# Performance work log

Measured on AMD Instinct MI355X. Metric: run time of the kernel, lower is better.

## Reference

```python
import jax, jax.numpy as jnp
import numpy as np

E, H, B, S = 512, 8, 8, 1024  # embed_dim, n_head, batch, n_agent (sequence)
DH = E // H
DECAY_SCALING = 1.0


def _rmsnorm(x, scale, eps=1e-6):
    return x * jax.lax.rsqrt(jnp.mean(x * x, axis=-1, keepdims=True) + eps) * scale


def _groupnorm(y, scale, bias, n_head, eps=1e-5):
    # GroupNorm with num_groups = n_head over the feature axis (flax semantics).
    b, s, e = y.shape
    yg = y.reshape(b, s, n_head, e // n_head)
    mu = jnp.mean(yg, axis=-1, keepdims=True)
    var = jnp.var(yg, axis=-1, keepdims=True)
    yn = (yg - mu) * jax.lax.rsqrt(var + eps)
    return yn.reshape(b, s, e) * scale + bias


def _decay_kappas(n_head, scaling):
    # RetNet multi-scale decays: 1 - exp(linspace(log(1/32), log(1/512), H))
    k = 1.0 - jnp.exp(jnp.linspace(jnp.log(1.0 / 32.0), jnp.log(1.0 / 512.0), n_head))
    return (k * scaling).astype(jnp.float32)


def _msr(key_x, query_x, value_x, wq, wk, wv, wg, wo, gs, gb, kappas):
    # Parallel multi-scale retention (masked / causal, full_self_retention=False).
    b, s, e = query_x.shape
    h = wq.shape[0]
    q = jnp.einsum('bse,hed->bhsd', query_x, wq)
    k = jnp.einsum('bse,hed->bhsd', key_x, wk)
    v = jnp.einsum('bse,hed->bhsd', value_x, wv)
    n = jnp.arange(s)
    diff = n[:, None] - n[None, :]
    causal = diff >= 0
    expnt = jnp.where(causal, diff, 0).astype(q.dtype)
    # D[h,n,m] = kappa_h^(n-m) for n>=m else 0
    D = jnp.where(causal[None], kappas[:, None, None] ** expnt[None], 0.0)
    scores = jnp.einsum('bhnd,bhmd->bhnm', q, k) * D[None]  # [B,H,S,S]
    ret = jnp.einsum('bhnm,bhmd->bhnd', scores, v)
    ret = ret.transpose(0, 2, 1, 3).reshape(b, s, e)
    ret = _groupnorm(ret, gs, gb, h)
    return (jax.nn.swish(query_x @ wg) * ret) @ wo


def _swiglu(x, w_gate, w_lin, w_out):
    return (jax.nn.swish(x @ w_gate) * (x @ w_lin)) @ w_out


def setup_inputs() -> dict:
    key = jax.random.key(0)
    ks = jax.random.split(key, 20)
    sc = 0.02
    d = {
        'x': jax.random.normal(ks[0], (B, S, E), jnp.float32),
        'obs_rep': jax.random.normal(ks[1], (B, S, E), jnp.float32),
        # retention 1 params
        'wq1': jax.random.normal(ks[2], (H, E, DH), jnp.float32) * sc,
        'wk1': jax.random.normal(ks[3], (H, E, DH), jnp.float32) * sc,
        'wv1': jax.random.normal(ks[4], (H, E, DH), jnp.float32) * sc,
        'wg1': jax.random.normal(ks[5], (E, E), jnp.float32) * sc,
        'wo1': jax.random.normal(ks[6], (E, E), jnp.float32) * sc,
        'gs1': jnp.ones((E,), jnp.float32),
        'gb1': jnp.zeros((E,), jnp.float32),
        # retention 2 params
        'wq2': jax.random.normal(ks[7], (H, E, DH), jnp.float32) * sc,
        'wk2': jax.random.normal(ks[8], (H, E, DH), jnp.float32) * sc,
        'wv2': jax.random.normal(ks[9], (H, E, DH), jnp.float32) * sc,
        'wg2': jax.random.normal(ks[10], (E, E), jnp.float32) * sc,
        'wo2': jax.random.normal(ks[11], (E, E), jnp.float32) * sc,
        'gs2': jnp.ones((E,), jnp.float32),
        'gb2': jnp.zeros((E,), jnp.float32),
        # RMSNorm scales
        'ln1_s': jnp.ones((E,), jnp.float32),
        'ln2_s': jnp.ones((E,), jnp.float32),
        'ln3_s': jnp.ones((E,), jnp.float32),
        # SwiGLU(hidden=E, input=E)
        'ffn_w_lin': jax.random.normal(ks[12], (E, E), jnp.float32) * sc,
        'ffn_w_gate': jax.random.normal(ks[13], (E, E), jnp.float32) * sc,
        'ffn_w_out': jax.random.normal(ks[14], (E, E), jnp.float32) * sc,
    }
    return d


def reference(x, obs_rep, wq1, wk1, wv1, wg1, wo1, gs1, gb1,
              wq2, wk2, wv2, wg2, wo2, gs2, gb2,
              ln1_s, ln2_s, ln3_s, ffn_w_lin, ffn_w_gate, ffn_w_out):
    kappas = _decay_kappas(H, DECAY_SCALING)
    # x = ln1(x + retn1(key=x, query=x, value=x))
    x1 = _rmsnorm(x + _msr(x, x, x, wq1, wk1, wv1, wg1, wo1, gs1, gb1, kappas), ln1_s)
    # x = ln2(obs_rep + retn2(key=x1, query=obs_rep, value=x1))
    x2 = _rmsnorm(obs_rep + _msr(x1, obs_rep, x1, wq2, wk2, wv2, wg2, wo2, gs2, gb2, kappas), ln2_s)
    # out = ln3(x2 + ffn(x2))
    return _rmsnorm(x2 + _swiglu(x2, ffn_w_gate, ffn_w_lin, ffn_w_out), ln3_s)
```

## Files before the change

### kernel.cpp

```cpp
#include <hip/hip_runtime.h>
#include <hip/hip_bf16.h>
#include <stdint.h>

typedef unsigned short u16;
typedef unsigned int   u32;
typedef __bf16 bf16x8 __attribute__((ext_vector_type(8)));
typedef u16    u16x8  __attribute__((ext_vector_type(8)));
typedef float  f32x4  __attribute__((ext_vector_type(4)));

#define E_   512
#define H_   8
#define DH_  64
#define B_   8
#define S_   1024
#define M_   (B_ * S_)
#define NTOT (M_ * E_)

__device__ __forceinline__ u16 f2bf(float f) {
    u32 x = __float_as_uint(f);
    x += 0x7fffu + ((x >> 16) & 1u);
    return (u16)(x >> 16);
}
__device__ __forceinline__ float bf2f(u16 b) { return __uint_as_float((u32)b << 16); }
__device__ __forceinline__ bf16x8 as_bf(u16x8 v) {
    union { u16x8 u; bf16x8 b; } x; x.u = v; return x.b;
}
__device__ __forceinline__ u32 cvtpk(float lo, float hi) {
    u32 r;
    asm("v_cvt_pk_bf16_f32 %0, %1, %2" : "=v"(r) : "v"(lo), "v"(hi));
    return r;
}
__device__ __forceinline__ void gll16(const u16* g, u16* l) {
    __builtin_amdgcn_global_load_lds((const __attribute__((address_space(1))) u32*)g,
                                     (__attribute__((address_space(3))) u32*)l, 16, 0, 0);
}
__device__ __forceinline__ void xcd_map(int f, int nwg, int gx, int& bx, int& by) {
    int nf = (f & 7) * (nwg >> 3) + (f >> 3);
    bx = nf % gx; by = nf / gx;
}

__global__ __launch_bounds__(256) void prep_weights(
    const float* __restrict__ wq1, const float* __restrict__ wk1, const float* __restrict__ wv1,
    const float* __restrict__ wg1, const float* __restrict__ wq2, const float* __restrict__ wk2,
    const float* __restrict__ wv2, const float* __restrict__ wg2, const float* __restrict__ wgat,
    const float* __restrict__ wlin, const float* __restrict__ wo1, const float* __restrict__ wo2,
    const float* __restrict__ wout,
    u16* __restrict__ WC1, u16* __restrict__ WC2, u16* __restrict__ WF,
    u16* __restrict__ WO1t, u16* __restrict__ WO2t, u16* __restrict__ WOUt) {
    __shared__ float tle[64][65];
    const int rt = blockIdx.y, c0 = blockIdx.x * 64, tid = threadIdx.x;
    u16* dst; const float* src; int lr0; bool qkv = false; int nb0 = 0, h = 0;
    if (rt < 64) {
        bool s1 = rt < 32;
        dst = s1 ? WC1 : WC2;
        int r = (rt & 31) * 64; lr0 = r;
        if (r < 1536) {
            qkv = true; h = (r >> 6) & 7;
            src = (r < 512) ? (s1 ? wq1 : wq2) : (r < 1024) ? (s1 ? wk1 : wk2) : (s1 ? wv1 : wv2);
        } else { src = s1 ? wg1 : wg2; nb0 = r - 1536; }
    } else if (rt < 80) {
        dst = WF; int r = (rt - 64) * 64; lr0 = r;
        src = (r < 512) ? wgat : wlin; nb0 = r & 511;
    } else if (rt < 88) { dst = WO1t; lr0 = (rt - 80) * 64; src = wo1; nb0 = lr0; }
    else if (rt < 96)   { dst = WO2t; lr0 = (rt - 88) * 64; src = wo2; nb0 = lr0; }
    else                { dst = WOUt; lr0 = (rt - 96) * 64; src = wout; nb0 = lr0; }

    #pragma unroll
    for (int i = 0; i < 16; ++i) {
        int idx = i * 256 + tid, a = idx >> 6, b = idx & 63;
        tle[a][b] = qkv ? src[(size_t)(h * 512 + c0 + a) * 64 + b]
                        : src[(size_t)(c0 + a) * 512 + nb0 + b];
    }
    __syncthreads();
    #pragma unroll
    for (int i = 0; i < 16; ++i) {
        int idx = i * 256 + tid;
        dst[(size_t)(lr0 + (idx >> 6)) * 512 + c0 + (idx & 63)] = f2bf(tle[idx & 63][idx >> 6]);
    }
}

__global__ __launch_bounds__(256) void cvt_both(const float* __restrict__ x,
                                                const float* __restrict__ obs,
                                                u16* __restrict__ XB, u16* __restrict__ OB) {
    int i = blockIdx.x * 256 + threadIdx.x;
    float4 v = ((const float4*)x)[i];
    ushort4 o;
    o.x = f2bf(v.x); o.y = f2bf(v.y); o.z = f2bf(v.z); o.w = f2bf(v.w);
    ((ushort4*)XB)[i] = o;
    v = ((const float4*)obs)[i];
    o.x = f2bf(v.x); o.y = f2bf(v.y); o.z = f2bf(v.z); o.w = f2bf(v.w);
    ((ushort4*)OB)[i] = o;
}

__global__ __launch_bounds__(256) void gemm_qkvg(const u16* __restrict__ A1,
                                                 const u16* __restrict__ A2,
                                                 const u16* __restrict__ W,
                                                 u16* __restrict__ QB, u16* __restrict__ KB,
                                                 u16* __restrict__ VT, u16* __restrict__ GB) {
    __shared__ u16 Als[128 * 64];
    __shared__ u16 Bls[128 * 64];
    const int tid = threadIdx.x;
    const int l = tid & 63, w = tid >> 6;
    const int wm = w & 1, wn = w >> 1;
    int bx, by; xcd_map(blockIdx.x, 1024, 16, bx, by);
    const int bm = by * 128, bn = bx * 128;
    const int which = bx >> 2;
    const u16* A = (which == 1 || which == 2) ? A2 : A1;

    size_t srcA[4], srcB[4]; int ldst[4];
    #pragma unroll
    for (int c = 0; c < 4; ++c) {
        int row = c * 32 + w * 8 + (l >> 3);
        int chs = (l & 7) ^ (row & 7);
        srcA[c] = (size_t)(bm + row) * E_ + chs * 8;
        srcB[c] = (size_t)(bn + row) * E_ + chs * 8;
        ldst[c] = c * 2048 + w * 512;
    }
    int aoff[2][4], boff[2][4];
    #pragma unroll
    for (int kk = 0; kk < 2; ++kk)
        #pragma unroll
        for (int f = 0; f < 4; ++f) {
            int ra = wm * 64 + f * 16 + (l & 15);
            int rb = wn * 64 + f * 16 + (l & 15);
            int ch = kk * 4 + (l >> 4);
            aoff[kk][f] = ra * 128 + ((ch ^ (ra & 7)) << 4);
            boff[kk][f] = rb * 128 + ((ch ^ (rb & 7)) << 4);
        }

    f32x4 acc[4][4] = {};
    for (int t = 0; t < 8; ++t) {
        const int k1 = t * 64;
        #pragma unroll
        for (int c = 0; c < 4; ++c) {
            gll16(A + srcA[c] + k1, &Als[ldst[c]]);
            gll16(W + srcB[c] + k1, &Bls[ldst[c]]);
        }
        __syncthreads();
        #pragma unroll
        for (int kk = 0; kk < 2; ++kk) {
            bf16x8 af[4], bfr[4];
            #pragma unroll
            for (int f = 0; f < 4; ++f) {
                af[f]  = as_bf(*(const u16x8*)((const char*)Als + aoff[kk][f]));
                bfr[f] = as_bf(*(const u16x8*)((const char*)Bls + boff[kk][f]));
            }
            #pragma unroll
            for (int m = 0; m < 4; ++m)
                #pragma unroll
                for (int n = 0; n < 4; ++n)
                    acc[m][n] = __builtin_amdgcn_mfma_f32_16x16x32_bf16(af[m], bfr[n], acc[m][n], 0, 0, 0);
        }
        __syncthreads();
    }

    #pragma unroll
    for (int m = 0; m < 4; ++m) {
        int row = bm + wm * 64 + m * 16 + ((l >> 4) << 2);
        #pragma unroll
        for (int n = 0; n < 4; ++n) {
            int coll = (bn & 511) + wn * 64 + n * 16 + (l & 15);
            f32x4 v = acc[m][n];
            if (which == 2) {
                size_t va = (((size_t)(row >> 10) * 8 + (coll >> 6)) * 64 + (coll & 63)) * 1024
                            + (row & 1023);
                ushort4 o;
                o.x = f2bf(v[0]); o.y = f2bf(v[1]); o.z = f2bf(v[2]); o.w = f2bf(v[3]);
                *(ushort4*)(VT + va) = o;
            } else {
                u16* dst = (which == 0) ? QB : (which == 1) ? KB : GB;
                #pragma unroll
                for (int r = 0; r < 4; ++r) dst[(size_t)(row + r) * E_ + coll] = f2bf(v[r]);
            }
        }
    }
}

__global__ __launch_bounds__(256) void gemm_wo(const u16* __restrict__ A,
                                               const u16* __restrict__ W,
                                               float* __restrict__ Cf) {
    __shared__ u16 Als[64 * 64];
    __shared__ u16 Bls[128 * 64];
    const int tid = threadIdx.x;
    const int l = tid & 63, w = tid >> 6;
    const int wm = w & 1, wn = w >> 1;
    int bx, by; xcd_map(blockIdx.x, 512, 4, bx, by);
    const int bm = by * 64, bn = bx * 128;

    size_t srcA[2], srcB[4]; int ldstA[2], ldstB[4];
    #pragma unroll
    for (int c = 0; c < 4; ++c) {
        int row = c * 32 + w * 8 + (l >> 3);
        int chs = (l & 7) ^ (row & 7);
        if (c < 2) { srcA[c] = (size_t)(bm + row) * E_ + chs * 8; ldstA[c] = c * 2048 + w * 512; }
        srcB[c] = (size_t)(bn + row) * E_ + chs * 8;
        ldstB[c] = c * 2048 + w * 512;
    }
    int aoff[2][2], boff[2][4];
    #pragma unroll
    for (int kk = 0; kk < 2; ++kk) {
        #pragma unroll
        for (int f = 0; f < 2; ++f) {
            int ra = wm * 32 + f * 16 + (l & 15);
            aoff[kk][f] = ra * 128 + (((kk * 4 + (l >> 4)) ^ (ra & 7)) << 4);
        }
        #pragma unroll
        for (int f = 0; f < 4; ++f) {
            int rb = wn * 64 + f * 16 + (l & 15);
            boff[kk][f] = rb * 128 + (((kk * 4 + (l >> 4)) ^ (rb & 7)) << 4);
        }
    }

    f32x4 acc[2][4] = {};
    for (int t = 0; t < 8; ++t) {
        const int k1 = t * 64;
        #pragma unroll
        for (int c = 0; c < 2; ++c) gll16(A + srcA[c] + k1, &Als[ldstA[c]]);
        #pragma unroll
        for (int c = 0; c < 4; ++c) gll16(W + srcB[c] + k1, &Bls[ldstB[c]]);
        __syncthreads();
        #pragma unroll
        for (int kk = 0; kk < 2; ++kk) {
            bf16x8 af[2], bfr[4];
            #pragma unroll
            for (int f = 0; f < 2; ++f) af[f] = as_bf(*(const u16x8*)((const char*)Als + aoff[kk][f]));
            #pragma unroll
            for (int f = 0; f < 4; ++f) bfr[f] = as_bf(*(const u16x8*)((const char*)Bls + boff[kk][f]));
            #pragma unroll
            for (int m = 0; m < 2; ++m)
                #pragma unroll
                for (int n = 0; n < 4; ++n)
                    acc[m][n] = __builtin_amdgcn_mfma_f32_16x16x32_bf16(af[m], bfr[n], acc[m][n], 0, 0, 0);
        }
        __syncthreads();
    }

    #pragma unroll
    for (int m = 0; m < 2; ++m) {
        int row = bm + wm * 32 + m * 16 + ((l >> 4) << 2);
        #pragma unroll
        for (int n = 0; n < 4; ++n) {
            int col = bn + wn * 64 + n * 16 + (l & 15);
            f32x4 v = acc[m][n];
            #pragma unroll
            for (int r = 0; r < 4; ++r) Cf[(size_t)(row + r) * E_ + col] = v[r];
        }
    }
}

__global__ __launch_bounds__(256) void gemm_ffn(const u16* __restrict__ A,
                                                const u16* __restrict__ W,
                                                u16* __restrict__ T) {
    __shared__ u16 Als[64 * 64];
    __shared__ u16 Bgs[64 * 64];
    __shared__ u16 Bls[64 * 64];
    const int tid = threadIdx.x;
    const int l = tid & 63, w = tid >> 6;
    const int wm = w & 1, wn = w >> 1;
    int bx, by; xcd_map(blockIdx.x, 1024, 8, bx, by);
    const int bm = by * 64, bn = bx * 64;

    size_t srcA[2], srcG[2], srcL[2]; int ldst[2];
    #pragma unroll
    for (int c = 0; c < 2; ++c) {
        int row = c * 32 + w * 8 + (l >> 3);
        int chs = (l & 7) ^ (row & 7);
        srcA[c] = (size_t)(bm + row) * E_ + chs * 8;
        srcG[c] = (size_t)(bn + row) * E_ + chs * 8;
        srcL[c] = (size_t)(512 + bn + row) * E_ + chs * 8;
        ldst[c] = c * 2048 + w * 512;
    }
    int aoff[2][2], goff[2][2];
    #pragma unroll
    for (int kk = 0; kk < 2; ++kk)
        #pragma unroll
        for (int f = 0; f < 2; ++f) {
            int ra = wm * 32 + f * 16 + (l & 15);
            int rb = wn * 32 + f * 16 + (l & 15);
            aoff[kk][f] = ra * 128 + (((kk * 4 + (l >> 4)) ^ (ra & 7)) << 4);
            goff[kk][f] = rb * 128 + (((kk * 4 + (l >> 4)) ^ (rb & 7)) << 4);
        }

    f32x4 accg[2][2] = {}, accl[2][2] = {};
    for (int t = 0; t < 8; ++t) {
        const int k1 = t * 64;
        #pragma unroll
        for (int c = 0; c < 2; ++c) {
            gll16(A + srcA[c] + k1, &Als[ldst[c]]);
            gll16(W + srcG[c] + k1, &Bgs[ldst[c]]);
            gll16(W + srcL[c] + k1, &Bls[ldst[c]]);
        }
        __syncthreads();
        #pragma unroll
        for (int kk = 0; kk < 2; ++kk) {
            bf16x8 af[2], bg[2], bl[2];
            #pragma unroll
            for (int f = 0; f < 2; ++f) {
                af[f] = as_bf(*(const u16x8*)((const char*)Als + aoff[kk][f]));
                bg[f] = as_bf(*(const u16x8*)((const char*)Bgs + goff[kk][f]));
                bl[f] = as_bf(*(const u16x8*)((const char*)Bls + goff[kk][f]));
            }
            #pragma unroll
            for (int m = 0; m < 2; ++m)
                #pragma unroll
                for (int n = 0; n < 2; ++n) {
                    accg[m][n] = __builtin_amdgcn_mfma_f32_16x16x32_bf16(af[m], bg[n], accg[m][n], 0, 0, 0);
                    accl[m][n] = __builtin_amdgcn_mfma_f32_16x16x32_bf16(af[m], bl[n], accl[m][n], 0, 0, 0);
                }
        }
        __syncthreads();
    }

    #pragma unroll
    for (int m = 0; m < 2; ++m) {
        int row = bm + wm * 32 + m * 16 + ((l >> 4) << 2);
        #pragma unroll
        for (int n = 0; n < 2; ++n) {
            int col = bn + wn * 32 + n * 16 + (l & 15);
            #pragma unroll
            for (int r = 0; r < 4; ++r) {
                float g = accg[m][n][r], lv = accl[m][n][r];
                T[(size_t)(row + r) * E_ + col] = f2bf(g * lv / (1.f + __expf(-g)));
            }
        }
    }
}

__global__ __launch_bounds__(256) void retention_fused(
        const u16* __restrict__ Q, const u16* __restrict__ K,
        const u16* __restrict__ VT, const u16* __restrict__ G,
        const float* __restrict__ gs, const float* __restrict__ gb,
        u16* __restrict__ T) {
    __shared__ u16 Qs[128 * 64], Ks[128 * 64], Vts[64 * 128], Ps[128 * 128];
    const int tid = threadIdx.x;
    const int l = tid & 63, w = tid >> 6;
    int id = blockIdx.x, nb, bh;
    if (id < 256) { nb = id & 7; bh = id >> 3; }
    else { int j = id - 256; nb = 7 - (j & 7); bh = 32 + (j >> 3); }
    const int h = bh & 7;
    const int n0 = nb * 128;
    const size_t base = (size_t)(bh >> 3) * (S_ * E_) + h * DH_;

    const float kappa = 1.0f - __expf(-3.46573590f + (float)h * -0.39608410f);
    const float log2k = log2f(kappa);
    const float ik = 1.0f / kappa;
    const float ikp2 = ik * ik, ikp3 = ik * ik * ik;

    float gsv[4], gbv[4];
    #pragma unroll
    for (int fd = 0; fd < 4; ++fd) {
        gsv[fd] = gs[h * 64 + fd * 16 + (l & 15)];
        gbv[fd] = gb[h * 64 + fd * 16 + (l & 15)];
    }

    {
        #pragma unroll
        for (int c = 0; c < 4; ++c) {
            int row = c * 32 + w * 8 + (l >> 3);
            int chs = (l & 7) ^ (row & 7);
            gll16(Q + base + (size_t)(n0 + row) * E_ + chs * 8, &Qs[c * 2048 + w * 512]);
        }
    }
    __syncthreads();
    bf16x8 qf[2][2];
    #pragma unroll
    for (int kk = 0; kk < 2; ++kk)
        #pragma unroll
        for (int fn = 0; fn < 2; ++fn) {
            int row = w * 32 + fn * 16 + (l & 15);
            int ch = kk * 4 + (l >> 4);
            qf[kk][fn] = as_bf(*(const u16x8*)((const char*)Qs + row * 128 + ((ch ^ (row & 7)) << 4)));
        }

    f32x4 acc[2][4] = {};
    const int nmin = n0 + w * 32;
    const int nmax = nmin + 31;

    for (int t = 0; t <= nb; ++t) {
        const int m0 = t * 128;
        __syncthreads();
        #pragma unroll
        for (int c = 0; c < 4; ++c) {
            int row = c * 32 + w * 8 + (l >> 3);
            int chs = (l & 7) ^ (row & 7);
            gll16(K + base + (size_t)(m0 + row) * E_ + chs * 8, &Ks[c * 2048 + w * 512]);
            int d = c * 16 + w * 4 + (l >> 4);
            int vch = (l & 15) ^ (d & 7);
            gll16(VT + ((size_t)bh * 64 + d) * 1024 + m0 + vch * 8, &Vts[c * 2048 + w * 512]);
        }
        __syncthreads();
        if (m0 > nmax) continue;
        const bool inter = (nmin >= m0 + 127);

        #pragma unroll
        for (int fmh = 0; fmh < 2; ++fmh) {
            bf16x8 kf[2][4];
            #pragma unroll
            for (int kk = 0; kk < 2; ++kk)
                #pragma unroll
                for (int f = 0; f < 4; ++f) {
                    int row = (fmh * 4 + f) * 16 + (l & 15);
                    int ch = kk * 4 + (l >> 4);
                    kf[kk][f] = as_bf(*(const u16x8*)((const char*)Ks + row * 128 + ((ch ^ (row & 7)) << 4)));
                }
            f32x4 s[4][2] = {};
            __builtin_amdgcn_s_setprio(1);
            #pragma unroll
            for (int kk = 0; kk < 2; ++kk)
                #pragma unroll
                for (int f = 0; f < 4; ++f)
                    #pragma unroll
                    for (int fn = 0; fn < 2; ++fn)
                        s[f][fn] = __builtin_amdgcn_mfma_f32_16x16x32_bf16(kf[kk][f], qf[kk][fn], s[f][fn], 0, 0, 0);
            __builtin_amdgcn_s_setprio(0);

            #pragma unroll
            for (int f = 0; f < 4; ++f) {
                int fm = fmh * 4 + f;
                #pragma unroll
                for (int fn = 0; fn < 2; ++fn) {
                    int n_g  = n0 + w * 32 + fn * 16 + (l & 15);
                    int mb_g = m0 + fm * 16 + ((l >> 4) << 2);
                    int delta = n_g - mb_g;
                    float wb = exp2f((float)delta * log2k);
                    f32x4 v = s[f][fn];
                    float p0, p1, p2, p3;
                    if (inter) {
                        float w1 = wb * ik, w2 = w1 * ik, w3 = w2 * ik;
                        p0 = v[0] * wb; p1 = v[1] * w1; p2 = v[2] * w2; p3 = v[3] * w3;
                    } else {
                        p0 = (delta >= 0) ? v[0] * wb : 0.f;
                        p1 = (delta >= 1) ? v[1] * wb * ik : 0.f;
                        p2 = (delta >= 2) ? v[2] * wb * ikp2 : 0.f;
                        p3 = (delta >= 3) ? v[3] * wb * ikp3 : 0.f;
                    }
                    int nl  = w * 32 + fn * 16 + (l & 15);
                    int mbl = fm * 16 + ((l >> 4) << 2);
                    int byteoff = nl * 256 + ((((mbl >> 3)) ^ (nl & 7)) << 4) + ((mbl & 4) << 1);
                    uint2 pk;
                    pk.x = cvtpk(p0, p1);
                    pk.y = cvtpk(p2, p3);
                    *(uint2*)((char*)Ps + byteoff) = pk;
                }
            }
        }

        #pragma unroll
        for (int km = 0; km < 4; ++km) {
            bf16x8 pf[2];
            #pragma unroll
            for (int fn = 0; fn < 2; ++fn) {
                int row = w * 32 + fn * 16 + (l & 15);
                int ch = km * 4 + (l >> 4);
                pf[fn] = as_bf(*(const u16x8*)((const char*)Ps + row * 256 + ((ch ^ (row & 7)) << 4)));
            }
            __builtin_amdgcn_s_setprio(1);
            #pragma unroll
            for (int fd = 0; fd < 4; ++fd) {
                int d = fd * 16 + (l & 15);
                int mch = km * 4 + (l >> 4);
                bf16x8 vfr = as_bf(*(const u16x8*)((const char*)Vts + d * 256 + ((mch ^ (d & 7)) << 4)));
                #pragma unroll
                for (int fn = 0; fn < 2; ++fn)
                    acc[fn][fd] = __builtin_amdgcn_mfma_f32_16x16x32_bf16(pf[fn], vfr, acc[fn][fd], 0, 0, 0);
            }
            __builtin_amdgcn_s_setprio(0);
        }
    }

    #pragma unroll
    for (int fn = 0; fn < 2; ++fn) {
        #pragma unroll
        for (int r = 0; r < 4; ++r) {
            float s1 = 0.f, s2 = 0.f;
            #pragma unroll
            for (int fd = 0; fd < 4; ++fd) { float v = acc[fn][fd][r]; s1 += v; s2 += v * v; }
            #pragma unroll
            for (int off = 1; off < 16; off <<= 1) {
                s1 += __shfl_xor(s1, off, 64);
                s2 += __shfl_xor(s2, off, 64);
            }
            float mean = s1 * (1.f / 64.f);
            float var  = s2 * (1.f / 64.f) - mean * mean;
            float rinv = rsqrtf(var + 1e-5f);
            int rowg = n0 + w * 32 + fn * 16 + ((l >> 4) << 2) + r;
            size_t rb = base + (size_t)rowg * E_;
            #pragma unroll
            for (int fd = 0; fd < 4; ++fd) {
                int d = fd * 16 + (l & 15);
                float ny = (acc[fn][fd][r] - mean) * rinv;
                float rn = ny * gsv[fd] + gbv[fd];
                float g = bf2f(G[rb + d]);
                T[rb + d] = f2bf(g * rn / (1.f + __expf(-g)));
            }
        }
    }
}

__global__ __launch_bounds__(512) void rmsnorm_res(const float* __restrict__ Xf,
                                                   const u16* __restrict__ Xb,
                                                   const float* __restrict__ Y,
                                                   const float* __restrict__ sc,
                                                   float* __restrict__ outf,
                                                   u16* __restrict__ outb) {
    __shared__ float part[8];
    size_t row = blockIdx.x;
    int t = threadIdx.x;
    float xv = Xf ? Xf[row * E_ + t] : bf2f(Xb[row * E_ + t]);
    float v = xv + Y[row * E_ + t];
    float sq = v * v;
    #pragma unroll
    for (int off = 1; off < 64; off <<= 1) sq += __shfl_xor(sq, off, 64);
    if ((t & 63) == 0) part[t >> 6] = sq;
    __syncthreads();
    float tot = 0.0f;
    #pragma unroll
    for (int i = 0; i < 8; ++i) tot += part[i];
    float r = rsqrtf(tot * (1.0f / 512.0f) + 1e-6f);
    float o = v * r * sc[t];
    if (outf) outf[row * E_ + t] = o;
    if (outb) outb[row * E_ + t] = f2bf(o);
}

extern "C" void kernel_launch(void* const* d_in, const int* in_sizes, int n_in,
                              void* d_out, int out_size, void* d_ws, size_t ws_size,
                              hipStream_t stream) {
    const float* x    = (const float*)d_in[0];
    const float* obs  = (const float*)d_in[1];
    const float* wq1  = (const float*)d_in[2];
    const float* wk1  = (const float*)d_in[3];
    const float* wv1  = (const float*)d_in[4];
    const float* wg1  = (const float*)d_in[5];
    const float* wo1  = (const float*)d_in[6];
    const float* gs1  = (const float*)d_in[7];
    const float* gb1  = (const float*)d_in[8];
    const float* wq2  = (const float*)d_in[9];
    const float* wk2  = (const float*)d_in[10];
    const float* wv2  = (const float*)d_in[11];
    const float* wg2  = (const float*)d_in[12];
    const float* wo2  = (const float*)d_in[13];
    const float* gs2  = (const float*)d_in[14];
    const float* gb2  = (const float*)d_in[15];
    const float* ln1s = (const float*)d_in[16];
    const float* ln2s = (const float*)d_in[17];
    const float* ln3s = (const float*)d_in[18];
    const float* wlin = (const float*)d_in[19];
    const float* wgat = (const float*)d_in[20];
    const float* wout = (const float*)d_in[21];

    u16* wsb = (u16*)d_ws;
    u16* WC1  = wsb;
    u16* WC2  = WC1 + 2048 * 512;
    u16* WF   = WC2 + 2048 * 512;
    u16* WO1t = WF + 1024 * 512;
    u16* WO2t = WO1t + 512 * 512;
    u16* WOUt = WO2t + 512 * 512;
    u16* XB   = WOUt + 512 * 512;
    u16* OB   = XB + NTOT;
    u16* QB   = OB + NTOT;
    u16* KB   = QB + NTOT;
    u16* VT   = KB + NTOT;
    u16* GB   = VT + NTOT;
    u16* TB   = GB + NTOT;
    float* GF = (float*)QB;

    dim3 tG(256);

    prep_weights<<<dim3(8, 104), tG, 0, stream>>>(wq1, wk1, wv1, wg1, wq2, wk2, wv2, wg2,
                                                  wgat, wlin, wo1, wo2, wout,
                                                  WC1, WC2, WF, WO1t, WO2t, WOUt);
    cvt_both<<<NTOT / 1024, tG, 0, stream>>>(x, obs, XB, OB);

    gemm_qkvg<<<1024, tG, 0, stream>>>(XB, XB, WC1, QB, KB, VT, GB);
    retention_fused<<<512, tG, 0, stream>>>(QB, KB, VT, GB, gs1, gb1, TB);
    gemm_wo<<<512, tG, 0, stream>>>(TB, WO1t, GF);
    rmsnorm_res<<<M_, 512, 0, stream>>>(x, nullptr, GF, ln1s, nullptr, XB);

    gemm_qkvg<<<1024, tG, 0, stream>>>(OB, XB, WC2, QB, KB, VT, GB);
    retention_fused<<<512, tG, 0, stream>>>(QB, KB, VT, GB, gs2, gb2, TB);
    gemm_wo<<<512, tG, 0, stream>>>(TB, WO2t, GF);
    rmsnorm_res<<<M_, 512, 0, stream>>>(obs, nullptr, GF, ln2s, nullptr, OB);

    gemm_ffn<<<1024, tG, 0, stream>>>(OB, WF, TB);
    gemm_wo<<<512, tG, 0, stream>>>(TB, WOUt, GF);
    rmsnorm_res<<<M_, 512, 0, stream>>>(nullptr, OB, GF, ln3s, (float*)d_out, nullptr);
}
```

Before: 210.9 us.

## Replace quadratic causal retention with chunkwise recurrent state formulation

Switches retention from the parallel form, which loops over all preceding 128-row key/value tiles, to a chunkwise form. A new kernel computes per-chunk decayed K^T V states, and each output chunk combines the decay-weighted sum of earlier states with an intra-chunk causal block. The QKV GEMM now also writes a transposed copy of K for the state kernel. This cuts the per-block work imbalance and the quadratic cost, but adds an extra launch, extra workspace traffic, and bf16 rounding of the inter-chunk states.

```diff
diff --git a/kernel.cpp b/kernel.cpp
--- a/kernel.cpp
+++ b/kernel.cpp
@@ -96,7 +96,8 @@
                                                  const u16* __restrict__ A2,
                                                  const u16* __restrict__ W,
                                                  u16* __restrict__ QB, u16* __restrict__ KB,
-                                                 u16* __restrict__ VT, u16* __restrict__ GB) {
+                                                 u16* __restrict__ KT, u16* __restrict__ VT,
+                                                 u16* __restrict__ GB) {
     __shared__ u16 Als[128 * 64];
     __shared__ u16 Bls[128 * 64];
     const int tid = threadIdx.x;
@@ -161,16 +162,281 @@
         for (int n = 0; n < 4; ++n) {
             int coll = (bn & 511) + wn * 64 + n * 16 + (l & 15);
             f32x4 v = acc[m][n];
+            size_t va = (((size_t)(row >> 10) * 8 + (coll >> 6)) * 64 + (coll & 63)) * 1024
+                        + (row & 1023);
             if (which == 2) {
-                size_t va = (((size_t)(row >> 10) * 8 + (coll >> 6)) * 64 + (coll & 63)) * 1024
-                            + (row & 1023);
                 ushort4 o;
                 o.x = f2bf(v[0]); o.y = f2bf(v[1]); o.z = f2bf(v[2]); o.w = f2bf(v[3]);
                 *(ushort4*)(VT + va) = o;
+            } else if (which == 1) {
+                #pragma unroll
+                for (int r = 0; r < 4; ++r) KB[(size_t)(row + r) * E_ + coll] = f2bf(v[r]);
+                ushort4 o;
+                o.x = f2bf(v[0]); o.y = f2bf(v[1]); o.z = f2bf(v[2]); o.w = f2bf(v[3]);
+                *(ushort4*)(KT + va) = o;
             } else {
-                u16* dst = (which == 0) ? QB : (which == 1) ? KB : GB;
+                u16* dst = (which == 0) ? QB : GB;
                 #pragma unroll
                 for (int r = 0; r < 4; ++r) dst[(size_t)(row + r) * E_ + coll] = f2bf(v[r]);
+            }
+        }
+    }
+}
+
+__global__ __launch_bounds__(256) void state_u(const u16* __restrict__ KT,
+                                               const u16* __restrict__ VT,
+                                               u16* __restrict__ U) {
+    const int id = blockIdx.x;
+    const int bh = id >> 3, c = id & 7;
+    const int h = bh & 7;
+    const int l = threadIdx.x & 63, w = threadIdx.x >> 6;
+    const float kappa = 1.0f - __expf(-3.46573590f + (float)h * -0.39608410f);
+    const float log2k = log2f(kappa);
+    const float ik = 1.0f / kappa;
+
+    bf16x8 af[4];
+    {
+        size_t vbase = ((size_t)bh * 64 + (w * 16 + (l & 15))) * 1024 + c * 128 + ((l >> 4) << 3);
+        #pragma unroll
+        for (int kk = 0; kk < 4; ++kk)
+            af[kk] = as_bf(*(const u16x8*)(VT + vbase + kk * 32));
+    }
+
+    f32x4 acc[4] = {};
+    #pragma unroll
+    for (int fd = 0; fd < 4; ++fd) {
+        size_t kbase = ((size_t)bh * 64 + (fd * 16 + (l & 15))) * 1024 + c * 128 + ((l >> 4) << 3);
+        #pragma unroll
+        for (int kk = 0; kk < 4; ++kk) {
+            u16x8 kv = *(const u16x8*)(KT + kbase + kk * 32);
+            int mb = kk * 32 + ((l >> 4) << 3);
+            float wj = exp2f((float)(127 - mb) * log2k);
+            u16x8 kw;
+            #pragma unroll
+            for (int j = 0; j < 8; ++j) { kw[j] = f2bf(bf2f(kv[j]) * wj); wj *= ik; }
+            acc[fd] = __builtin_amdgcn_mfma_f32_16x16x32_bf16(af[kk], as_bf(kw), acc[fd], 0, 0, 0);
+        }
+    }
+
+    #pragma unroll
+    for (int fd = 0; fd < 4; ++fd) {
+        int dv = w * 16 + ((l >> 4) << 2);
+        int dk = fd * 16 + (l & 15);
+        size_t ub = ((size_t)id * 64 + dv) * 64 + dk;
+        #pragma unroll
+        for (int r = 0; r < 4; ++r) U[ub + (size_t)r * 64] = f2bf(acc[fd][r]);
+    }
+}
+
+__global__ __launch_bounds__(256) void retention_chunk(
+        const u16* __restrict__ Q, const u16* __restrict__ K,
+        const u16* __restrict__ VT, const u16* __restrict__ U,
+        const u16* __restrict__ G,
+        const float* __restrict__ gs, const float* __restrict__ gb,
+        u16* __restrict__ T) {
+    __shared__ u16 Ks[128 * 64], Vts[64 * 128], Ps[128 * 64], Ss[64 * 64];
+    const int tid = threadIdx.x;
+    const int l = tid & 63, w = tid >> 6;
+    const int id = blockIdx.x;
+    const int bh = id >> 3, c = id & 7;
+    const int h = bh & 7;
+    const int n0 = c * 128;
+    const size_t base = (size_t)(bh >> 3) * (S_ * E_) + h * DH_;
+
+    const float kappa = 1.0f - __expf(-3.46573590f + (float)h * -0.39608410f);
+    const float log2k = log2f(kappa);
+    const float ik = 1.0f / kappa;
+    const float ikp2 = ik * ik, ikp3 = ikp2 * ik;
+
+    float gsv[4], gbv[4];
+    #pragma unroll
+    for (int fd = 0; fd < 4; ++fd) {
+        gsv[fd] = gs[h * 64 + fd * 16 + (l & 15)];
+        gbv[fd] = gb[h * 64 + fd * 16 + (l & 15)];
+    }
+
+    #pragma unroll
+    for (int cc = 0; cc < 4; ++cc) {
+        int row = cc * 32 + w * 8 + (l >> 3);
+        int chs = (l & 7) ^ (row & 7);
+        gll16(K + base + (size_t)(n0 + row) * E_ + chs * 8, &Ks[cc * 2048 + w * 512]);
+        int d = cc * 16 + w * 4 + (l >> 4);
+        int vch = (l & 15) ^ (d & 15);
+        gll16(VT + ((size_t)bh * 64 + d) * 1024 + n0 + vch * 8, &Vts[cc * 2048 + w * 512]);
+    }
+
+    bf16x8 qf[2][2];
+    #pragma unroll
+    for (int kk = 0; kk < 2; ++kk)
+        #pragma unroll
+        for (int fn = 0; fn < 2; ++fn) {
+            int n = n0 + fn * 64 + w * 16 + (l & 15);
+            qf[kk][fn] = as_bf(*(const u16x8*)(Q + base + (size_t)n * E_ + kk * 32 + ((l >> 4) << 3)));
+        }
+
+    if (c > 0) {
+        float accs[16];
+        #pragma unroll
+        for (int j = 0; j < 16; ++j) accs[j] = 0.f;
+        const float kC = exp2f(128.0f * log2k);
+        float wc = 1.0f;
+        size_t ub = (size_t)bh * (8 * 4096) + tid * 16;
+        for (int cp = c - 1; cp >= 0; --cp) {
+            const u16* up = U + ub + (size_t)cp * 4096;
+            u16x8 a = *(const u16x8*)up;
+            u16x8 b = *(const u16x8*)(up + 8);
+            #pragma unroll
+            for (int j = 0; j < 8; ++j) {
+                accs[j]     += bf2f(a[j]) * wc;
+                accs[8 + j] += bf2f(b[j]) * wc;
+            }
+            wc *= kC;
+        }
+        int dv = tid >> 2, ch0 = (tid & 3) << 1;
+        #pragma unroll
+        for (int hh = 0; hh < 2; ++hh) {
+            uint4 pk;
+            pk.x = cvtpk(accs[hh * 8 + 0], accs[hh * 8 + 1]);
+            pk.y = cvtpk(accs[hh * 8 + 2], accs[hh * 8 + 3]);
+            pk.z = cvtpk(accs[hh * 8 + 4], accs[hh * 8 + 5]);
+            pk.w = cvtpk(accs[hh * 8 + 6], accs[hh * 8 + 7]);
+            *(uint4*)((char*)Ss + dv * 128 + (((ch0 + hh) ^ (dv & 7)) << 4)) = pk;
+        }
+    }
+    __syncthreads();
+
+    f32x4 acc[2][4] = {};
+
+    if (c > 0) {
+        __builtin_amdgcn_s_setprio(1);
+        #pragma unroll
+        for (int kk = 0; kk < 2; ++kk) {
+            bf16x8 sf[4];
+            #pragma unroll
+            for (int fd = 0; fd < 4; ++fd) {
+                int dv = fd * 16 + (l & 15);
+                int ch = kk * 4 + (l >> 4);
+                sf[fd] = as_bf(*(const u16x8*)((const char*)Ss + dv * 128 + ((ch ^ (dv & 7)) << 4)));
+            }
+            #pragma unroll
+            for (int fn = 0; fn < 2; ++fn)
+                #pragma unroll
+                for (int fd = 0; fd < 4; ++fd)
+                    acc[fn][fd] = __builtin_amdgcn_mfma_f32_16x16x32_bf16(qf[kk][fn], sf[fd], acc[fn][fd], 0, 0, 0);
+        }
+        __builtin_amdgcn_s_setprio(0);
+        #pragma unroll
+        for (int fn = 0; fn < 2; ++fn) {
+            int nl0 = fn * 64 + w * 16 + ((l >> 4) << 2);
+            float fr0 = exp2f((float)(nl0 + 1) * log2k);
+            float fr1 = fr0 * kappa, fr2 = fr1 * kappa, fr3 = fr2 * kappa;
+            #pragma unroll
+            for (int fd = 0; fd < 4; ++fd) {
+                acc[fn][fd][0] *= fr0; acc[fn][fd][1] *= fr1;
+                acc[fn][fd][2] *= fr2; acc[fn][fd][3] *= fr3;
+            }
+        }
+    }
+
+    #pragma unroll
+    for (int mh = 0; mh < 2; ++mh) {
+        const int m0l = mh * 64;
+        bf16x8 kf[2][4];
+        #pragma unroll
+        for (int kk = 0; kk < 2; ++kk)
+            #pragma unroll
+            for (int f = 0; f < 4; ++f) {
+                int row = m0l + f * 16 + (l & 15);
+                int ch = kk * 4 + (l >> 4);
+                kf[kk][f] = as_bf(*(const u16x8*)((const char*)Ks + row * 128 + ((ch ^ (row & 7)) << 4)));
+            }
+        #pragma unroll
+        for (int fn = 0; fn < 2; ++fn) {
+            if (mh == 1 && fn == 0) continue;
+            f32x4 s[4] = {};
+            __builtin_amdgcn_s_setprio(1);
+            #pragma unroll
+            for (int kk = 0; kk < 2; ++kk)
+                #pragma unroll
+                for (int f = 0; f < 4; ++f)
+                    s[f] = __builtin_amdgcn_mfma_f32_16x16x32_bf16(kf[kk][f], qf[kk][fn], s[f], 0, 0, 0);
+            __builtin_amdgcn_s_setprio(0);
+            const bool fast = (mh == 0 && fn == 1);
+            int nl = fn * 64 + w * 16 + (l & 15);
+            #pragma unroll
+            for (int f = 0; f < 4; ++f) {
+                int mbl = m0l + f * 16 + ((l >> 4) << 2);
+                int delta = nl - mbl;
+                float wb = exp2f((float)delta * log2k);
+                f32x4 v = s[f];
+                float p0, p1, p2, p3;
+                if (fast) {
+                    float w1 = wb * ik, w2 = w1 * ik, w3 = w2 * ik;
+                    p0 = v[0] * wb; p1 = v[1] * w1; p2 = v[2] * w2; p3 = v[3] * w3;
+                } else {
+                    p0 = (delta >= 0) ? v[0] * wb : 0.f;
+                    p1 = (delta >= 1) ? v[1] * wb * ik : 0.f;
+                    p2 = (delta >= 2) ? v[2] * wb * ikp2 : 0.f;
+                    p3 = (delta >= 3) ? v[3] * wb * ikp3 : 0.f;
+                }
+                int mcl = f * 16 + ((l >> 4) << 2);
+                int byteoff = nl * 128 + (((mcl >> 3) ^ (nl & 7)) << 4) + ((mcl & 4) << 1);
+                uint2 pk;
+                pk.x = cvtpk(p0, p1);
+                pk.y = cvtpk(p2, p3);
+                *(uint2*)((char*)Ps + byteoff) = pk;
+            }
+        }
+        #pragma unroll
+        for (int km = 0; km < 2; ++km) {
+            bf16x8 pf[2];
+            #pragma unroll
+            for (int fn = 0; fn < 2; ++fn) {
+                if (mh == 1 && fn == 0) continue;
+                int row = fn * 64 + w * 16 + (l & 15);
+                int ch = km * 4 + (l >> 4);
+                pf[fn] = as_bf(*(const u16x8*)((const char*)Ps + row * 128 + ((ch ^ (row & 7)) << 4)));
+            }
+            __builtin_amdgcn_s_setprio(1);
+            #pragma unroll
+            for (int fd = 0; fd < 4; ++fd) {
+                int d = fd * 16 + (l & 15);
+                int mch = mh * 8 + km * 4 + (l >> 4);
+                bf16x8 vfr = as_bf(*(const u16x8*)((const char*)Vts + d * 256 + ((mch ^ (d & 15)) << 4)));
+                #pragma unroll
+                for (int fn = 0; fn < 2; ++fn) {
+                    if (mh == 1 && fn == 0) continue;
+                    acc[fn][fd] = __builtin_amdgcn_mfma_f32_16x16x32_bf16(pf[fn], vfr, acc[fn][fd], 0, 0, 0);
+                }
+            }
+            __builtin_amdgcn_s_setprio(0);
+        }
+    }
+
+    #pragma unroll
+    for (int fn = 0; fn < 2; ++fn) {
+        #pragma unroll
+        for (int r = 0; r < 4; ++r) {
+            float s1 = 0.f, s2 = 0.f;
+            #pragma unroll
+            for (int fd = 0; fd < 4; ++fd) { float v = acc[fn][fd][r]; s1 += v; s2 += v * v; }
+            #pragma unroll
+            for (int off = 1; off < 16; off <<= 1) {
+                s1 += __shfl_xor(s1, off, 64);
+                s2 += __shfl_xor(s2, off, 64);
+            }
+            float mean = s1 * (1.f / 64.f);
+            float var  = s2 * (1.f / 64.f) - mean * mean;
+            float rinv = rsqrtf(var + 1e-5f);
+            int rowg = n0 + fn * 64 + w * 16 + ((l >> 4) << 2) + r;
+            size_t rb = base + (size_t)rowg * E_;
+            #pragma unroll
+            for (int fd = 0; fd < 4; ++fd) {
+                int d = fd * 16 + (l & 15);
+                float ny = (acc[fn][fd][r] - mean) * rinv;
+                float rn = ny * gsv[fd] + gbv[fd];
+                float g = bf2f(G[rb + d]);
+                T[rb + d] = f2bf(g * rn / (1.f + __expf(-g)));
             }
         }
     }
@@ -321,177 +587,6 @@
             for (int r = 0; r < 4; ++r) {
                 float g = accg[m][n][r], lv = accl[m][n][r];
                 T[(size_t)(row + r) * E_ + col] = f2bf(g * lv / (1.f + __expf(-g)));
-            }
-        }
-    }
-}
-
-__global__ __launch_bounds__(256) void retention_fused(
-        const u16* __restrict__ Q, const u16* __restrict__ K,
-        const u16* __restrict__ VT, const u16* __restrict__ G,
-        const float* __restrict__ gs, const float* __restrict__ gb,
-        u16* __restrict__ T) {
-    __shared__ u16 Qs[128 * 64], Ks[128 * 64], Vts[64 * 128], Ps[128 * 128];
-    const int tid = threadIdx.x;
-    const int l = tid & 63, w = tid >> 6;
-    int id = blockIdx.x, nb, bh;
-    if (id < 256) { nb = id & 7; bh = id >> 3; }
-    else { int j = id - 256; nb = 7 - (j & 7); bh = 32 + (j >> 3); }
-    const int h = bh & 7;
-    const int n0 = nb * 128;
-    const size_t base = (size_t)(bh >> 3) * (S_ * E_) + h * DH_;
-
-    const float kappa = 1.0f - __expf(-3.46573590f + (float)h * -0.39608410f);
-    const float log2k = log2f(kappa);
-    const float ik = 1.0f / kappa;
-    const float ikp2 = ik * ik, ikp3 = ik * ik * ik;
-
-    float gsv[4], gbv[4];
-    #pragma unroll
-    for (int fd = 0; fd < 4; ++fd) {
-        gsv[fd] = gs[h * 64 + fd * 16 + (l & 15)];
-        gbv[fd] = gb[h * 64 + fd * 16 + (l & 15)];
-    }
-
-    {
-        #pragma unroll
-        for (int c = 0; c < 4; ++c) {
-            int row = c * 32 + w * 8 + (l >> 3);
-            int chs = (l & 7) ^ (row & 7);
-            gll16(Q + base + (size_t)(n0 + row) * E_ + chs * 8, &Qs[c * 2048 + w * 512]);
-        }
-    }
-    __syncthreads();
-    bf16x8 qf[2][2];
-    #pragma unroll
-    for (int kk = 0; kk < 2; ++kk)
-        #pragma unroll
-        for (int fn = 0; fn < 2; ++fn) {
-            int row = w * 32 + fn * 16 + (l & 15);
-            int ch = kk * 4 + (l >> 4);
-            qf[kk][fn] = as_bf(*(const u16x8*)((const char*)Qs + row * 128 + ((ch ^ (row & 7)) << 4)));
-        }
-
-    f32x4 acc[2][4] = {};
-    const int nmin = n0 + w * 32;
-    const int nmax = nmin + 31;
-
-    for (int t = 0; t <= nb; ++t) {
-        const int m0 = t * 128;
-        __syncthreads();
-        #pragma unroll
-        for (int c = 0; c < 4; ++c) {
-            int row = c * 32 + w * 8 + (l >> 3);
-            int chs = (l & 7) ^ (row & 7);
-            gll16(K + base + (size_t)(m0 + row) * E_ + chs * 8, &Ks[c * 2048 + w * 512]);
-            int d = c * 16 + w * 4 + (l >> 4);
-            int vch = (l & 15) ^ (d & 7);
-            gll16(VT + ((size_t)bh * 64 + d) * 1024 + m0 + vch * 8, &Vts[c * 2048 + w * 512]);
-        }
-        __syncthreads();
-        if (m0 > nmax) continue;
-        const bool inter = (nmin >= m0 + 127);
-
-        #pragma unroll
-        for (int fmh = 0; fmh < 2; ++fmh) {
-            bf16x8 kf[2][4];
-            #pragma unroll
-            for (int kk = 0; kk < 2; ++kk)
-                #pragma unroll
-                for (int f = 0; f < 4; ++f) {
-                    int row = (fmh * 4 + f) * 16 + (l & 15);
-                    int ch = kk * 4 + (l >> 4);
-                    kf[kk][f] = as_bf(*(const u16x8*)((const char*)Ks + row * 128 + ((ch ^ (row & 7)) << 4)));
-                }
-            f32x4 s[4][2] = {};
-            __builtin_amdgcn_s_setprio(1);
-            #pragma unroll
-            for (int kk = 0; kk < 2; ++kk)
-                #pragma unroll
-                for (int f = 0; f < 4; ++f)
-                    #pragma unroll
-                    for (int fn = 0; fn < 2; ++fn)
-                        s[f][fn] = __builtin_amdgcn_mfma_f32_16x16x32_bf16(kf[kk][f], qf[kk][fn], s[f][fn], 0, 0, 0);
-            __builtin_amdgcn_s_setprio(0);
-
-            #pragma unroll
-            for (int f = 0; f < 4; ++f) {
-                int fm = fmh * 4 + f;
-                #pragma unroll
-                for (int fn = 0; fn < 2; ++fn) {
-                    int n_g  = n0 + w * 32 + fn * 16 + (l & 15);
-                    int mb_g = m0 + fm * 16 + ((l >> 4) << 2);
-                    int delta = n_g - mb_g;
-                    float wb = exp2f((float)delta * log2k);
-                    f32x4 v = s[f][fn];
-                    float p0, p1, p2, p3;
-                    if (inter) {
-                        float w1 = wb * ik, w2 = w1 * ik, w3 = w2 * ik;
-                        p0 = v[0] * wb; p1 = v[1] * w1; p2 = v[2] * w2; p3 = v[3] * w3;
-                    } else {
-                        p0 = (delta >= 0) ? v[0] * wb : 0.f;
-                        p1 = (delta >= 1) ? v[1] * wb * ik : 0.f;
-                        p2 = (delta >= 2) ? v[2] * wb * ikp2 : 0.f;
-                        p3 = (delta >= 3) ? v[3] * wb * ikp3 : 0.f;
-                    }
-                    int nl  = w * 32 + fn * 16 + (l & 15);
-                    int mbl = fm * 16 + ((l >> 4) << 2);
-                    int byteoff = nl * 256 + ((((mbl >> 3)) ^ (nl & 7)) << 4) + ((mbl & 4) << 1);
-                    uint2 pk;
-                    pk.x = cvtpk(p0, p1);
-                    pk.y = cvtpk(p2, p3);
-                    *(uint2*)((char*)Ps + byteoff) = pk;
-                }
-            }
-        }
-
-        #pragma unroll
-        for (int km = 0; km < 4; ++km) {
-            bf16x8 pf[2];
-            #pragma unroll
-            for (int fn = 0; fn < 2; ++fn) {
-                int row = w * 32 + fn * 16 + (l & 15);
-                int ch = km * 4 + (l >> 4);
-                pf[fn] = as_bf(*(const u16x8*)((const char*)Ps + row * 256 + ((ch ^ (row & 7)) << 4)));
-            }
-            __builtin_amdgcn_s_setprio(1);
-            #pragma unroll
-            for (int fd = 0; fd < 4; ++fd) {
-                int d = fd * 16 + (l & 15);
-                int mch = km * 4 + (l >> 4);
-                bf16x8 vfr = as_bf(*(const u16x8*)((const char*)Vts + d * 256 + ((mch ^ (d & 7)) << 4)));
-                #pragma unroll
-                for (int fn = 0; fn < 2; ++fn)
-                    acc[fn][fd] = __builtin_amdgcn_mfma_f32_16x16x32_bf16(pf[fn], vfr, acc[fn][fd], 0, 0, 0);
-            }
-            __builtin_amdgcn_s_setprio(0);
-        }
-    }
-
-    #pragma unroll
-    for (int fn = 0; fn < 2; ++fn) {
-        #pragma unroll
-        for (int r = 0; r < 4; ++r) {
-            float s1 = 0.f, s2 = 0.f;
-            #pragma unroll
-            for (int fd = 0; fd < 4; ++fd) { float v = acc[fn][fd][r]; s1 += v; s2 += v * v; }
-            #pragma unroll
-            for (int off = 1; off < 16; off <<= 1) {
-                s1 += __shfl_xor(s1, off, 64);
-                s2 += __shfl_xor(s2, off, 64);
-            }
-            float mean = s1 * (1.f / 64.f);
-            float var  = s2 * (1.f / 64.f) - mean * mean;
-            float rinv = rsqrtf(var + 1e-5f);
-            int rowg = n0 + w * 32 + fn * 16 + ((l >> 4) << 2) + r;
-            size_t rb = base + (size_t)rowg * E_;
-            #pragma unroll
-            for (int fd = 0; fd < 4; ++fd) {
-                int d = fd * 16 + (l & 15);
-                float ny = (acc[fn][fd][r] - mean) * rinv;
-                float rn = ny * gsv[fd] + gbv[fd];
-                float g = bf2f(G[rb + d]);
-                T[rb + d] = f2bf(g * rn / (1.f + __expf(-g)));
             }
         }
     }
@@ -559,9 +654,11 @@
     u16* OB   = XB + NTOT;
     u16* QB   = OB + NTOT;
     u16* KB   = QB + NTOT;
-    u16* VT   = KB + NTOT;
+    u16* KT   = KB + NTOT;
+    u16* VT   = KT + NTOT;
     u16* GB   = VT + NTOT;
     u16* TB   = GB + NTOT;
+    u16* UB   = TB + NTOT;
     float* GF = (float*)QB;
 
     dim3 tG(256);
@@ -571,13 +668,15 @@
                                                   WC1, WC2, WF, WO1t, WO2t, WOUt);
     cvt_both<<<NTOT / 1024, tG, 0, stream>>>(x, obs, XB, OB);
 
-    gemm_qkvg<<<1024, tG, 0, stream>>>(XB, XB, WC1, QB, KB, VT, GB);
-    retention_fused<<<512, tG, 0, stream>>>(QB, KB, VT, GB, gs1, gb1, TB);
+    gemm_qkvg<<<1024, tG, 0, stream>>>(XB, XB, WC1, QB, KB, KT, VT, GB);
+    state_u<<<512, tG, 0, stream>>>(KT, VT, UB);
+    retention_chunk<<<512, tG, 0, stream>>>(QB, KB, VT, UB, GB, gs1, gb1, TB);
     gemm_wo<<<512, tG, 0, stream>>>(TB, WO1t, GF);
     rmsnorm_res<<<M_, 512, 0, stream>>>(x, nullptr, GF, ln1s, nullptr, XB);
 
-    gemm_qkvg<<<1024, tG, 0, stream>>>(OB, XB, WC2, QB, KB, VT, GB);
-    retention_fused<<<512, tG, 0, stream>>>(QB, KB, VT, GB, gs2, gb2, TB);
+    gemm_qkvg<<<1024, tG, 0, stream>>>(OB, XB, WC2, QB, KB, KT, VT, GB);
+    state_u<<<512, tG, 0, stream>>>(KT, VT, UB);
+    retention_chunk<<<512, tG, 0, stream>>>(QB, KB, VT, UB, GB, gs2, gb2, TB);
     gemm_wo<<<512, tG, 0, stream>>>(TB, WO2t, GF);
     rmsnorm_res<<<M_, 512, 0, stream>>>(obs, nullptr, GF, ln2s, nullptr, OB);
 
```

Measured after the change: 203.6 us. -3.4%, faster.
